# Kernel tuning notes

Measured on AMD Instinct MI355X. Metric: run time of the kernel, lower is better.

Reference implementation:

```python
import jax, jax.numpy as jnp
import numpy as np

EMBED_DIM = 768
NUM_HEADS = 12
HEAD_DIM = EMBED_DIM // NUM_HEADS
BSZ = 2
SEQ = 2048


def setup_inputs() -> dict:
    key = jax.random.key(0)
    ks = jax.random.split(key, 8)
    w = lambda k: (jax.random.normal(k, (EMBED_DIM, EMBED_DIM), jnp.float32) * 0.02)
    return {
        "hidden_states": jax.random.normal(ks[0], (BSZ, SEQ, EMBED_DIM), jnp.float32),
        "attention_mask": jnp.zeros((BSZ, 1, SEQ, SEQ), jnp.float32),
        "attention_bias": jax.random.normal(ks[1], (BSZ * NUM_HEADS, SEQ), jnp.float32),
        "Wq": w(ks[2]), "bq": jnp.zeros((EMBED_DIM,), jnp.float32),
        "Wk": w(ks[3]), "bk": jnp.zeros((EMBED_DIM,), jnp.float32),
        "Wv": w(ks[4]), "bv": jnp.zeros((EMBED_DIM,), jnp.float32),
        "Wo": w(ks[5]), "bo": jnp.zeros((EMBED_DIM,), jnp.float32),
        "beta": jnp.ones((1,), jnp.float32),
        "beta_bias": jnp.zeros((1,), jnp.float32),
    }


def reference(hidden_states, attention_mask, attention_bias, Wq, bq, Wk, bk, Wv, bv, Wo, bo, beta, beta_bias):
    b, t, e = hidden_states.shape
    scaling = HEAD_DIM ** -0.5
    split = lambda x: x.reshape(b, t, NUM_HEADS, HEAD_DIM).transpose(0, 2, 1, 3)  # b h t d
    q = split(hidden_states @ Wq.T + bq) * scaling
    k = split(hidden_states @ Wk.T + bk)
    v = split(hidden_states @ Wv.T + bv)
    # scores: [b, h, t, s]
    scores = jnp.einsum('bhqd,bhkd->bhqk', q, k)
    bias = attention_bias.reshape(b, NUM_HEADS, 1, t)  # (bsz*nh, src) -> broadcast over queries
    scores = scores + beta * bias + beta_bias + attention_mask
    probs = jax.nn.softmax(scores, axis=-1)
    out = jnp.einsum('bhqk,bhkd->bhqd', probs, v)  # b h t d
    out = out.transpose(0, 2, 1, 3).reshape(b, t, e)
    return out @ Wo.T + bo
```

## Files before the change

### kernel.cpp

```cpp
#include <hip/hip_runtime.h>
#include <hip/hip_bf16.h>

#define E 768
#define HD 64
#define NH 12
#define BSZ 2
#define SEQ 2048
#define M_ROWS (BSZ * SEQ)
#define BH (BSZ * NH)

#define LOG2E 1.44269504f
#define QSCALE 0.18033688f
#define MSHIFT 16.0f

typedef float f4_t __attribute__((ext_vector_type(4)));
typedef float f32x16 __attribute__((ext_vector_type(16)));
typedef __bf16 bf8_t __attribute__((ext_vector_type(8)));
typedef unsigned short us8_t __attribute__((ext_vector_type(8)));
typedef unsigned short us4_t __attribute__((ext_vector_type(4)));

__device__ inline unsigned short f2bf(float f) {
  union { float f; unsigned u; } v; v.f = f;
  unsigned u = v.u + 0x7FFFu + ((v.u >> 16) & 1u);
  return (unsigned short)(u >> 16);
}

__device__ inline float ex2(float x) { return __builtin_amdgcn_exp2f(x); }

__device__ inline float bflo(unsigned u) { union { unsigned u; float f; } v; v.u = u << 16; return v.f; }
__device__ inline float bfhi(unsigned u) { union { unsigned u; float f; } v; v.u = u & 0xFFFF0000u; return v.f; }

__device__ inline unsigned pk2(float a, float b) {
  union { float f; unsigned u; } ua, ub;
  ua.f = a; ub.f = b;
  return __builtin_amdgcn_perm(ub.u + 0x8000u, ua.u + 0x8000u, 0x07060302u);
}

__device__ inline void swap32(unsigned& a, unsigned& b) {
  asm volatile("v_permlane32_swap_b32 %0, %1" : "+v"(a), "+v"(b));
}

__global__ __launch_bounds__(256) void cvt_all(
    const float* __restrict__ X, const float* __restrict__ Wq,
    const float* __restrict__ Wk, const float* __restrict__ Wv,
    const float* __restrict__ Wo, const float* __restrict__ mask,
    const float* __restrict__ abias, const float* __restrict__ betaP,
    const float* __restrict__ bbiasP,
    unsigned short* __restrict__ Xbf, unsigned short* __restrict__ Wqkv,
    unsigned short* __restrict__ Wobf, unsigned short* __restrict__ maskbf,
    float* __restrict__ biasPf) {
  const int nW = E * E;
  int id = blockIdx.x;
  if (id < 2688) {
    const float* src;
    unsigned short* dst;
    float scale = 1.0f;
    int base;
    if (id < 1536) {
      src = X; dst = Xbf; base = id * 2048;
    } else {
      int r = id - 1536;
      int k = r / 288;
      int rb = r - k * 288;
      base = rb * 2048;
      if (k == 0)      { src = Wq; dst = Wqkv;          scale = QSCALE; }
      else if (k == 1) { src = Wk; dst = Wqkv + nW;     }
      else if (k == 2) { src = Wv; dst = Wqkv + 2 * nW; }
      else             { src = Wo; dst = Wobf;          }
    }
    int i = base + threadIdx.x * 8;
    const float4* s = (const float4*)(src + i);
    float4 a = s[0], b = s[1];
    us8_t o;
    o[0] = f2bf(a.x * scale); o[1] = f2bf(a.y * scale);
    o[2] = f2bf(a.z * scale); o[3] = f2bf(a.w * scale);
    o[4] = f2bf(b.x * scale); o[5] = f2bf(b.y * scale);
    o[6] = f2bf(b.z * scale); o[7] = f2bf(b.w * scale);
    *(us8_t*)(dst + i) = o;
    return;
  }
  if (id < 6784) {
    int rowid = id - 2688;
    int bb = rowid >> 11, q = rowid & 2047;
    int s0 = threadIdx.x * 8;
    const float4* s = (const float4*)(mask + (size_t)rowid * 2048 + s0);
    float4 a = s[0], c = s[1];
    int tile = s0 >> 6, kk = s0 & 63;
    int base = ((bb * 32 + tile) * 2048 + q) * 64 + (kk >> 5) * 32 + ((kk & 31) >> 3) * 4;
    us4_t lo, hi4;
    lo[0] = f2bf(a.x * LOG2E); lo[1] = f2bf(a.y * LOG2E);
    lo[2] = f2bf(a.z * LOG2E); lo[3] = f2bf(a.w * LOG2E);
    hi4[0] = f2bf(c.x * LOG2E); hi4[1] = f2bf(c.y * LOG2E);
    hi4[2] = f2bf(c.z * LOG2E); hi4[3] = f2bf(c.w * LOG2E);
    *(us4_t*)(maskbf + base) = lo;
    *(us4_t*)(maskbf + base + 16) = hi4;
    return;
  }
  {
    int bh = id - 6784;
    int s0 = threadIdx.x * 8;
    const float4* s = (const float4*)(abias + (size_t)bh * 2048 + s0);
    float4 a = s[0], c = s[1];
    float bv = LOG2E * betaP[0];
    float bc = LOG2E * bbiasP[0] - MSHIFT;
    int tile = s0 >> 6, kk = s0 & 63;
    int base = bh * 2048 + tile * 64 + (kk >> 5) * 32 + ((kk & 31) >> 3) * 4;
    f4_t lo = {fmaf(bv, a.x, bc), fmaf(bv, a.y, bc), fmaf(bv, a.z, bc), fmaf(bv, a.w, bc)};
    f4_t hi4 = {fmaf(bv, c.x, bc), fmaf(bv, c.y, bc), fmaf(bv, c.z, bc), fmaf(bv, c.w, bc)};
    *(f4_t*)(biasPf + base) = lo;
    *(f4_t*)(biasPf + base + 16) = hi4;
  }
}

__global__ __launch_bounds__(256) void gemm_qkv(
    const unsigned short* __restrict__ A, const unsigned short* __restrict__ Bw,
    const float* __restrict__ bq, const float* __restrict__ bk, const float* __restrict__ bv,
    unsigned short* __restrict__ Qb, unsigned short* __restrict__ Kb,
    unsigned short* __restrict__ Vtb) {
  __shared__ unsigned short Alds[2][64 * 64];
  __shared__ unsigned short Blds[2][128 * 64];
  const int w = threadIdx.x >> 6, lane = threadIdx.x & 63;
  const int quad = lane >> 4, l15 = lane & 15;
  const int rowBase = blockIdx.x * 64;
  const int colBase = blockIdx.y * 128;
  const int wr = (w & 1) * 32, wc = (w >> 1) * 64;
  f4_t acc[2][4] = {};
  const int swz = l15 & 7;

#define STAGE_QKV(BUF, K0)                                                       \
  {                                                                              \
    const int kk0_ = (K0);                                                       \
    for (int c = 0; c < 2; ++c) {                                                \
      int s = c * 256 + w * 64 + lane;                                           \
      int r = s >> 3, col = ((s & 7) ^ (r & 7)) * 8;                             \
      const unsigned short* ga = A + (size_t)(rowBase + r) * E + kk0_ + col;     \
      __builtin_amdgcn_global_load_lds(                                          \
          (const __attribute__((address_space(1))) void*)ga,                     \
          (__attribute__((address_space(3))) void*)&Alds[BUF][c * 2048 + w * 512], 16, 0, 0); \
    }                                                                            \
    for (int c = 0; c < 4; ++c) {                                                \
      int s = c * 256 + w * 64 + lane;                                           \
      int r = s >> 3, col = ((s & 7) ^ (r & 7)) * 8;                             \
      const unsigned short* gb = Bw + (size_t)(colBase + r) * E + kk0_ + col;    \
      __builtin_amdgcn_global_load_lds(                                          \
          (const __attribute__((address_space(1))) void*)gb,                     \
          (__attribute__((address_space(3))) void*)&Blds[BUF][c * 2048 + w * 512], 16, 0, 0); \
    }                                                                            \
  }

  STAGE_QKV(0, 0);
  __builtin_amdgcn_s_waitcnt(0);
  __syncthreads();
  for (int t = 0; t < 12; ++t) {
    const int cur = t & 1;
    if (t < 11) STAGE_QKV(cur ^ 1, (t + 1) * 64);
    bf8_t af[2][2], bfr[4][2];
#pragma unroll
    for (int mi = 0; mi < 2; ++mi)
#pragma unroll
      for (int ks = 0; ks < 2; ++ks)
        af[mi][ks] = *(const bf8_t*)&Alds[cur][(wr + mi * 16 + l15) * 64 + (((ks * 4 + quad) ^ swz) << 3)];
#pragma unroll
    for (int ni = 0; ni < 4; ++ni)
#pragma unroll
      for (int ks = 0; ks < 2; ++ks)
        bfr[ni][ks] = *(const bf8_t*)&Blds[cur][(wc + ni * 16 + l15) * 64 + (((ks * 4 + quad) ^ swz) << 3)];
#pragma unroll
    for (int ks = 0; ks < 2; ++ks)
#pragma unroll
      for (int mi = 0; mi < 2; ++mi)
#pragma unroll
        for (int ni = 0; ni < 4; ++ni)
          acc[mi][ni] = __builtin_amdgcn_mfma_f32_16x16x32_bf16(af[mi][ks], bfr[ni][ks], acc[mi][ni], 0, 0, 0);
    __builtin_amdgcn_s_waitcnt(0);
    __syncthreads();
  }
#undef STAGE_QKV

  const int which = colBase / E;
  if (which < 2) {
    const float* biasP = (which == 0) ? bq : bk;
    unsigned short* dst = (which == 0) ? Qb : Kb;
    const float bscale = (which == 0) ? QSCALE : 1.0f;
    const int cnBase = colBase - which * E + wc;
    const int h = cnBase >> 6;
    float biasv[4];
#pragma unroll
    for (int ni = 0; ni < 4; ++ni) biasv[ni] = biasP[cnBase + ni * 16 + l15] * bscale;
    unsigned short* T = &Blds[0][0] + w * 1024;
    const int row = lane >> 2, colE = (lane & 3) * 16;
#pragma unroll
    for (int mi = 0; mi < 2; ++mi) {
#pragma unroll
      for (int ni = 0; ni < 4; ++ni)
#pragma unroll
        for (int r = 0; r < 4; ++r)
          T[(quad * 4 + r) * 64 + ni * 16 + l15] = f2bf(acc[mi][ni][r] + biasv[ni]);
      us8_t o0 = *(const us8_t*)&T[row * 64 + colE];
      us8_t o1 = *(const us8_t*)&T[row * 64 + colE + 8];
      int gm = rowBase + wr + mi * 16 + row;
      int b = gm >> 11, t = gm & 2047;
      unsigned short* drow = dst + ((size_t)(b * NH + h) * SEQ + t) * HD;
      *(us8_t*)&drow[colE] = o0;
      *(us8_t*)&drow[colE + 8] = o1;
    }
  } else {
#pragma unroll
    for (int mi = 0; mi < 2; ++mi) {
#pragma unroll
      for (int ni = 0; ni < 4; ++ni) {
        int cn = colBase - 2 * E + wc + ni * 16 + l15;
        int h = cn >> 6, d = cn & 63;
        float bias = bv[cn];
        int gm0 = rowBase + wr + mi * 16 + quad * 4;
        int b = gm0 >> 11, t = gm0 & 2047;
        us4_t o4;
#pragma unroll
        for (int r = 0; r < 4; ++r) o4[r] = f2bf(acc[mi][ni][r] + bias);
        *(us4_t*)&Vtb[((size_t)(b * NH + h) * HD + d) * SEQ + t] = o4;
      }
    }
  }
}

__device__ inline void initS(f32x16& SA, const float* bp, us8_t ma, us8_t mb) {
  union { us8_t s; unsigned u[4]; } ca, cb;
  ca.s = ma; cb.s = mb;
#pragma unroll
  for (int g = 0; g < 4; ++g) {
    f4_t bw = *(const f4_t*)(bp + g * 4);
    unsigned wl = (g < 2) ? ca.u[2 * g] : cb.u[2 * g - 4];
    unsigned wh = (g < 2) ? ca.u[2 * g + 1] : cb.u[2 * g - 3];
    SA[4 * g + 0] = bw[0] + bflo(wl);
    SA[4 * g + 1] = bw[1] + bfhi(wl);
    SA[4 * g + 2] = bw[2] + bflo(wh);
    SA[4 * g + 3] = bw[3] + bfhi(wh);
  }
}

__device__ inline void packP(f32x16& SA, float& L, bf8_t& F0, bf8_t& F1) {
#pragma unroll
  for (int r = 0; r < 16; ++r) {
    SA[r] = ex2(SA[r]);
    L += SA[r];
  }
  unsigned u0 = pk2(SA[0], SA[1]), u1 = pk2(SA[2], SA[3]);
  unsigned u2 = pk2(SA[4], SA[5]), u3 = pk2(SA[6], SA[7]);
  unsigned u4 = pk2(SA[8], SA[9]), u5 = pk2(SA[10], SA[11]);
  unsigned u6 = pk2(SA[12], SA[13]), u7 = pk2(SA[14], SA[15]);
  swap32(u0, u2); swap32(u1, u3); swap32(u4, u6); swap32(u5, u7);
  union { unsigned u[4]; bf8_t b; } fa, fb;
  fa.u[0] = u0; fa.u[1] = u1; fa.u[2] = u2; fa.u[3] = u3;
  fb.u[0] = u4; fb.u[1] = u5; fb.u[2] = u6; fb.u[3] = u7;
  F0 = fa.b; F1 = fb.b;
}

__global__ __launch_bounds__(256, 3) void flash_attn15(
    const unsigned short* __restrict__ Qb, const unsigned short* __restrict__ Kb,
    const unsigned short* __restrict__ Vt, const unsigned short* __restrict__ maskP,
    const float* __restrict__ biasPf, unsigned short* __restrict__ attn) {
  __shared__ __align__(16) char smem[40960];
  const int tid = threadIdx.x;
  const int w = tid >> 6, lane = tid & 63;
  const int l31 = lane & 31, hi = lane >> 5;
  const int p = w >> 1, qw = (w & 1) * 32;
  const int id = blockIdx.x;
  const int h = id >> 6;
  const int qb = id & 63;
  const int qt = qb >> 1, b = qb & 1;
  const int bh = b * NH + h;
  const int q0 = qt * 64;
  const int q = q0 + qw + l31;

  unsigned short* KldsP = (unsigned short*)(smem + p * 16384);
  unsigned short* VldsP = KldsP + 4096;
  float* biasF = (float*)(smem + 32768);

  {
    const float* srcB = biasPf + bh * 2048 + tid * 8;
    *(f4_t*)&biasF[tid * 8] = *(const f4_t*)srcB;
    *(f4_t*)&biasF[tid * 8 + 4] = *(const f4_t*)(srcB + 4);
  }

  bf8_t qf[4];
  {
    const unsigned short* qbase = Qb + ((size_t)bh * SEQ + q) * HD + hi * 8;
#pragma unroll
    for (int dk = 0; dk < 4; ++dk) qf[dk] = *(const bf8_t*)(qbase + dk * 16);
  }

  const int li = (w & 1) * 64 + lane;
  const int r0 = li >> 3, cc = li & 7;
  const int dstOff = r0 * 64 + ((cc ^ (r0 & 7)) << 3);
  const unsigned short* kb0 = Kb + (size_t)bh * SEQ * HD + (p * 1024 + r0) * 64 + cc * 8;
  const unsigned short* VtG = Vt + (size_t)bh * HD * SEQ;
  const unsigned short* vb0 = VtG + (size_t)r0 * SEQ + p * 1024 + cc * 8;
  const unsigned short* mpp = maskP + (((size_t)(b * 32 + p * 16) * 2048) + q) * 64 + hi * 16;

  us8_t kpf0, kpf1, kpf2, kpf3, vpf0, vpf1, vpf2, vpf3, mpf0, mpf1, mpf2, mpf3;

#define PF_KV()                                                               \
  asm volatile("global_load_dwordx4 %0, %8, off\n\t"                          \
               "global_load_dwordx4 %1, %8, off offset:2048\n\t"              \
               "global_load_dwordx4 %2, %9, off\n\t"                          \
               "global_load_dwordx4 %3, %9, off offset:2048\n\t"              \
               "global_load_dwordx4 %4, %10, off\n\t"                         \
               "global_load_dwordx4 %5, %11, off\n\t"                         \
               "global_load_dwordx4 %6, %12, off\n\t"                         \
               "global_load_dwordx4 %7, %13, off"                             \
               : "=&v"(kpf0), "=&v"(kpf1), "=&v"(kpf2), "=&v"(kpf3),          \
                 "=&v"(vpf0), "=&v"(vpf1), "=&v"(vpf2), "=&v"(vpf3)           \
               : "v"(kb0), "v"(kb0 + 2048), "v"(vb0), "v"(vb0 + 16 * SEQ),    \
                 "v"(vb0 + 32 * SEQ), "v"(vb0 + 48 * SEQ))

#define PF_M()                                                                \
  asm volatile("global_load_dwordx4 %0, %4, off\n\t"                          \
               "global_load_dwordx4 %1, %4, off offset:16\n\t"                \
               "global_load_dwordx4 %2, %4, off offset:64\n\t"                \
               "global_load_dwordx4 %3, %4, off offset:80"                    \
               : "=&v"(mpf0), "=&v"(mpf1), "=&v"(mpf2), "=&v"(mpf3)           \
               : "v"(mpp))

  PF_KV();
  PF_M();

  f32x16 Oacc0 = {}, Oacc1 = {};
  float Lacc = 0.0f;
  const int swzA = l31 & 7;

  for (int it = 0; it < 16; ++it) {
    asm volatile("s_waitcnt vmcnt(4)"
                 : "+v"(kpf0), "+v"(kpf1), "+v"(kpf2), "+v"(kpf3),
                   "+v"(vpf0), "+v"(vpf1), "+v"(vpf2), "+v"(vpf3));
    __syncthreads();
    {
      us8_t* kd = (us8_t*)(KldsP + dstOff);
      kd[0] = kpf0; kd[128] = kpf1; kd[256] = kpf2; kd[384] = kpf3;
      us8_t* vd = (us8_t*)(VldsP + dstOff);
      vd[0] = vpf0; vd[128] = vpf1; vd[256] = vpf2; vd[384] = vpf3;
    }
    __syncthreads();

    if (it < 15) {
      kb0 += 4096; vb0 += 64;
      PF_KV();
      asm volatile("s_waitcnt vmcnt(8)"
                   : "+v"(mpf0), "+v"(mpf1), "+v"(mpf2), "+v"(mpf3));
    } else {
      asm volatile("s_waitcnt vmcnt(0)"
                   : "+v"(mpf0), "+v"(mpf1), "+v"(mpf2), "+v"(mpf3));
    }

    const float* bp = biasF + ((p << 4) + it) * 64 + (hi << 4);
    f32x16 s0, s1;
    initS(s0, bp, mpf0, mpf1);
    initS(s1, bp + 32, mpf2, mpf3);

    if (it < 15) { mpp += 131072; PF_M(); }

    __builtin_amdgcn_s_setprio(1);
#pragma unroll
    for (int dk = 0; dk < 4; ++dk) {
      const int co = ((dk * 2 + hi) ^ swzA) << 3;
      bf8_t k0 = *(const bf8_t*)(KldsP + l31 * 64 + co);
      bf8_t k1 = *(const bf8_t*)(KldsP + (32 + l31) * 64 + co);
      s0 = __builtin_amdgcn_mfma_f32_32x32x16_bf16(k0, qf[dk], s0, 0, 0, 0);
      s1 = __builtin_amdgcn_mfma_f32_32x32x16_bf16(k1, qf[dk], s1, 0, 0, 0);
    }
    __builtin_amdgcn_s_setprio(0);

    bf8_t pfr0, pfr1, pfr2, pfr3;
    packP(s0, Lacc, pfr0, pfr1);
    packP(s1, Lacc, pfr2, pfr3);

    __builtin_amdgcn_s_setprio(1);
#pragma unroll
    for (int ks = 0; ks < 4; ++ks) {
      const int co = ((ks * 2 + hi) ^ swzA) << 3;
      bf8_t v0 = *(const bf8_t*)(VldsP + l31 * 64 + co);
      bf8_t v1 = *(const bf8_t*)(VldsP + (32 + l31) * 64 + co);
      bf8_t pp = ks == 0 ? pfr0 : ks == 1 ? pfr1 : ks == 2 ? pfr2 : pfr3;
      Oacc0 = __builtin_amdgcn_mfma_f32_32x32x16_bf16(v0, pp, Oacc0, 0, 0, 0);
      Oacc1 = __builtin_amdgcn_mfma_f32_32x32x16_bf16(v1, pp, Oacc1, 0, 0, 0);
    }
    __builtin_amdgcn_s_setprio(0);
  }
#undef PF_KV
#undef PF_M

  __syncthreads();
  {
    float* OfP = (float*)smem + p * (64 * 65);
    const int qr = (qw + l31) * 65;
#pragma unroll
    for (int r = 0; r < 16; ++r) {
      int d = (r & 3) + 8 * (r >> 2) + 4 * hi;
      OfP[qr + d] = Oacc0[r];
      OfP[qr + 32 + d] = Oacc1[r];
    }
    float Lf = Lacc + __shfl_xor(Lacc, 32);
    if (hi == 0) OfP[qr + 64] = Lf;
  }
  __syncthreads();
  {
    const float* O0 = (const float*)smem;
    const float* O1 = O0 + 64 * 65;
    const int ql = tid >> 2, dc = tid & 3;
    const int qr = ql * 65;
    float inv = 1.0f / (O0[qr + 64] + O1[qr + 64]);
    unsigned short* orow = attn + ((size_t)b * SEQ + q0 + ql) * E + h * HD + dc * 16;
    us8_t o0, o1;
#pragma unroll
    for (int i = 0; i < 8; ++i)
      o0[i] = f2bf((O0[qr + dc * 16 + i] + O1[qr + dc * 16 + i]) * inv);
#pragma unroll
    for (int i = 0; i < 8; ++i)
      o1[i] = f2bf((O0[qr + dc * 16 + 8 + i] + O1[qr + dc * 16 + 8 + i]) * inv);
    *(us8_t*)orow = o0;
    *(us8_t*)(orow + 8) = o1;
  }
}

__global__ __launch_bounds__(256) void gemm_out(
    const unsigned short* __restrict__ A, const unsigned short* __restrict__ Bw,
    const float* __restrict__ bo, float* __restrict__ out) {
  __shared__ unsigned short Alds[2][64 * 64];
  __shared__ unsigned short Blds[2][64 * 64];
  const int w = threadIdx.x >> 6, lane = threadIdx.x & 63;
  const int quad = lane >> 4, l15 = lane & 15;
  const int rowBase = blockIdx.x * 64;
  const int colBase = blockIdx.y * 64;
  const int wr = (w & 1) * 32, wc = (w >> 1) * 32;
  f4_t acc[2][2] = {};
  const int swz = l15 & 7;

#define STAGE_OUT(BUF, K0)                                                       \
  {                                                                              \
    const int kk0_ = (K0);                                                       \
    for (int c = 0; c < 2; ++c) {                                                \
      int s = c * 256 + w * 64 + lane;                                           \
      int r = s >> 3, col = ((s & 7) ^ (r & 7)) * 8;                             \
      const unsigned short* ga = A + (size_t)(rowBase + r) * E + kk0_ + col;     \
      __builtin_amdgcn_global_load_lds(                                          \
          (const __attribute__((address_space(1))) void*)ga,                     \
          (__attribute__((address_space(3))) void*)&Alds[BUF][c * 2048 + w * 512], 16, 0, 0); \
      const unsigned short* gb = Bw + (size_t)(colBase + r) * E + kk0_ + col;    \
      __builtin_amdgcn_global_load_lds(                                          \
          (const __attribute__((address_space(1))) void*)gb,                     \
          (__attribute__((address_space(3))) void*)&Blds[BUF][c * 2048 + w * 512], 16, 0, 0); \
    }                                                                            \
  }

  STAGE_OUT(0, 0);
  __builtin_amdgcn_s_waitcnt(0);
  __syncthreads();
  for (int t = 0; t < 12; ++t) {
    const int cur = t & 1;
    if (t < 11) STAGE_OUT(cur ^ 1, (t + 1) * 64);
    bf8_t af[2][2], bfr[2][2];
#pragma unroll
    for (int mi = 0; mi < 2; ++mi)
#pragma unroll
      for (int ks = 0; ks < 2; ++ks)
        af[mi][ks] = *(const bf8_t*)&Alds[cur][(wr + mi * 16 + l15) * 64 + (((ks * 4 + quad) ^ swz) << 3)];
#pragma unroll
    for (int ni = 0; ni < 2; ++ni)
#pragma unroll
      for (int ks = 0; ks < 2; ++ks)
        bfr[ni][ks] = *(const bf8_t*)&Blds[cur][(wc + ni * 16 + l15) * 64 + (((ks * 4 + quad) ^ swz) << 3)];
#pragma unroll
    for (int ks = 0; ks < 2; ++ks)
#pragma unroll
      for (int mi = 0; mi < 2; ++mi)
#pragma unroll
        for (int ni = 0; ni < 2; ++ni)
          acc[mi][ni] = __builtin_amdgcn_mfma_f32_16x16x32_bf16(af[mi][ks], bfr[ni][ks], acc[mi][ni], 0, 0, 0);
    __builtin_amdgcn_s_waitcnt(0);
    __syncthreads();
  }
#undef STAGE_OUT

#pragma unroll
  for (int mi = 0; mi < 2; ++mi) {
#pragma unroll
    for (int ni = 0; ni < 2; ++ni) {
      int gn = colBase + wc + ni * 16 + l15;
      float bias = bo[gn];
#pragma unroll
      for (int r = 0; r < 4; ++r) {
        int gm = rowBase + wr + mi * 16 + quad * 4 + r;
        out[(size_t)gm * E + gn] = acc[mi][ni][r] + bias;
      }
    }
  }
}

extern "C" void kernel_launch(void* const* d_in, const int* in_sizes, int n_in,
                              void* d_out, int out_size, void* d_ws, size_t ws_size,
                              hipStream_t stream) {
  const float* hidden = (const float*)d_in[0];
  const float* mask = (const float*)d_in[1];
  const float* abias = (const float*)d_in[2];
  const float* Wq = (const float*)d_in[3];
  const float* bq = (const float*)d_in[4];
  const float* Wk = (const float*)d_in[5];
  const float* bk = (const float*)d_in[6];
  const float* Wv = (const float*)d_in[7];
  const float* bv = (const float*)d_in[8];
  const float* Wo = (const float*)d_in[9];
  const float* bo = (const float*)d_in[10];
  const float* beta = (const float*)d_in[11];
  const float* betaBias = (const float*)d_in[12];
  float* out = (float*)d_out;

  char* ws = (char*)d_ws;
  unsigned short* Xbf = (unsigned short*)(ws);
  unsigned short* Wqkv = (unsigned short*)(ws + 6291456);
  unsigned short* Wobf = (unsigned short*)(ws + 9830400);
  unsigned short* Qbuf = (unsigned short*)(ws + 11010048);
  unsigned short* Kbuf = (unsigned short*)(ws + 17301504);
  unsigned short* Vtb = (unsigned short*)(ws + 23592960);
  unsigned short* Maskbf = (unsigned short*)(ws + 29884416);
  float* BiasP = (float*)(ws + 46661632);
  unsigned short* Attn = Xbf;

  cvt_all<<<6808, 256, 0, stream>>>(hidden, Wq, Wk, Wv, Wo, mask, abias, beta, betaBias,
                                    Xbf, Wqkv, Wobf, Maskbf, BiasP);
  gemm_qkv<<<dim3(64, 18), 256, 0, stream>>>(Xbf, Wqkv, bq, bk, bv, Qbuf, Kbuf, Vtb);
  flash_attn15<<<768, 256, 0, stream>>>(Qbuf, Kbuf, Vtb, Maskbf, BiasP, Attn);
  gemm_out<<<dim3(64, 12), 256, 0, stream>>>(Attn, Wobf, bo, out);
}
```

Measured before the change: 200.8 us.

## Enlarge GEMM tiles, drop double buffering, and tree-reduce softmax row sums

The QKV GEMM moves from 64x128 to 128x128 tiles with 4x4 MFMA accumulators per wave and a minimum of 3 blocks per CU. The output GEMM moves from 64x64 to 64x128 tiles. Both GEMMs drop LDS double buffering for a single buffer with a sync before and after each load, which reuses each loaded tile more and cuts LDS use but stops overlapping loads with MFMA work. The softmax row sum in the attention kernel now uses a tree reduction instead of a serial chain, shortening the dependency chain.

```diff
diff --git a/kernel.cpp b/kernel.cpp
--- a/kernel.cpp
+++ b/kernel.cpp
@@ -112,85 +112,72 @@
   }
 }
 
-__global__ __launch_bounds__(256) void gemm_qkv(
+__global__ __launch_bounds__(256, 3) void gemm_qkv(
     const unsigned short* __restrict__ A, const unsigned short* __restrict__ Bw,
     const float* __restrict__ bq, const float* __restrict__ bk, const float* __restrict__ bv,
     unsigned short* __restrict__ Qb, unsigned short* __restrict__ Kb,
     unsigned short* __restrict__ Vtb) {
-  __shared__ unsigned short Alds[2][64 * 64];
-  __shared__ unsigned short Blds[2][128 * 64];
+  __shared__ unsigned short Alds[128 * 64];
+  __shared__ unsigned short Blds[128 * 64];
   const int w = threadIdx.x >> 6, lane = threadIdx.x & 63;
   const int quad = lane >> 4, l15 = lane & 15;
-  const int rowBase = blockIdx.x * 64;
+  const int rowBase = blockIdx.x * 128;
   const int colBase = blockIdx.y * 128;
-  const int wr = (w & 1) * 32, wc = (w >> 1) * 64;
-  f4_t acc[2][4] = {};
+  const int wr = (w & 1) * 64, wc = (w >> 1) * 64;
+  f4_t acc[4][4] = {};
   const int swz = l15 & 7;
 
-#define STAGE_QKV(BUF, K0)                                                       \
-  {                                                                              \
-    const int kk0_ = (K0);                                                       \
-    for (int c = 0; c < 2; ++c) {                                                \
-      int s = c * 256 + w * 64 + lane;                                           \
-      int r = s >> 3, col = ((s & 7) ^ (r & 7)) * 8;                             \
-      const unsigned short* ga = A + (size_t)(rowBase + r) * E + kk0_ + col;     \
-      __builtin_amdgcn_global_load_lds(                                          \
-          (const __attribute__((address_space(1))) void*)ga,                     \
-          (__attribute__((address_space(3))) void*)&Alds[BUF][c * 2048 + w * 512], 16, 0, 0); \
-    }                                                                            \
-    for (int c = 0; c < 4; ++c) {                                                \
-      int s = c * 256 + w * 64 + lane;                                           \
-      int r = s >> 3, col = ((s & 7) ^ (r & 7)) * 8;                             \
-      const unsigned short* gb = Bw + (size_t)(colBase + r) * E + kk0_ + col;    \
-      __builtin_amdgcn_global_load_lds(                                          \
-          (const __attribute__((address_space(1))) void*)gb,                     \
-          (__attribute__((address_space(3))) void*)&Blds[BUF][c * 2048 + w * 512], 16, 0, 0); \
-    }                                                                            \
-  }
-
-  STAGE_QKV(0, 0);
-  __builtin_amdgcn_s_waitcnt(0);
-  __syncthreads();
-  for (int t = 0; t < 12; ++t) {
-    const int cur = t & 1;
-    if (t < 11) STAGE_QKV(cur ^ 1, (t + 1) * 64);
-    bf8_t af[2][2], bfr[4][2];
-#pragma unroll
-    for (int mi = 0; mi < 2; ++mi)
+  for (int k0 = 0; k0 < E; k0 += 64) {
+    __syncthreads();
+#pragma unroll
+    for (int c = 0; c < 4; ++c) {
+      int s = c * 256 + w * 64 + lane;
+      int r = s >> 3, col = ((s & 7) ^ (r & 7)) * 8;
+      const unsigned short* ga = A + (size_t)(rowBase + r) * E + k0 + col;
+      __builtin_amdgcn_global_load_lds((const __attribute__((address_space(1))) void*)ga,
+          (__attribute__((address_space(3))) void*)&Alds[c * 2048 + w * 512], 16, 0, 0);
+      const unsigned short* gb = Bw + (size_t)(colBase + r) * E + k0 + col;
+      __builtin_amdgcn_global_load_lds((const __attribute__((address_space(1))) void*)gb,
+          (__attribute__((address_space(3))) void*)&Blds[c * 2048 + w * 512], 16, 0, 0);
+    }
+    __builtin_amdgcn_s_waitcnt(0);
+    __syncthreads();
+    bf8_t af[4][2], bfr[4][2];
+#pragma unroll
+    for (int mi = 0; mi < 4; ++mi)
 #pragma unroll
       for (int ks = 0; ks < 2; ++ks)
-        af[mi][ks] = *(const bf8_t*)&Alds[cur][(wr + mi * 16 + l15) * 64 + (((ks * 4 + quad) ^ swz) << 3)];
+        af[mi][ks] = *(const bf8_t*)&Alds[(wr + mi * 16 + l15) * 64 + (((ks * 4 + quad) ^ swz) << 3)];
 #pragma unroll
     for (int ni = 0; ni < 4; ++ni)
 #pragma unroll
       for (int ks = 0; ks < 2; ++ks)
-        bfr[ni][ks] = *(const bf8_t*)&Blds[cur][(wc + ni * 16 + l15) * 64 + (((ks * 4 + quad) ^ swz) << 3)];
+        bfr[ni][ks] = *(const bf8_t*)&Blds[(wc + ni * 16 + l15) * 64 + (((ks * 4 + quad) ^ swz) << 3)];
 #pragma unroll
     for (int ks = 0; ks < 2; ++ks)
 #pragma unroll
-      for (int mi = 0; mi < 2; ++mi)
+      for (int mi = 0; mi < 4; ++mi)
 #pragma unroll
         for (int ni = 0; ni < 4; ++ni)
           acc[mi][ni] = __builtin_amdgcn_mfma_f32_16x16x32_bf16(af[mi][ks], bfr[ni][ks], acc[mi][ni], 0, 0, 0);
-    __builtin_amdgcn_s_waitcnt(0);
-    __syncthreads();
-  }
-#undef STAGE_QKV
-
-  const int which = colBase / E;
+  }
+
+  const int which = blockIdx.y / 6;
+  const int colMat = colBase - which * E;
+  __syncthreads();
   if (which < 2) {
     const float* biasP = (which == 0) ? bq : bk;
     unsigned short* dst = (which == 0) ? Qb : Kb;
     const float bscale = (which == 0) ? QSCALE : 1.0f;
-    const int cnBase = colBase - which * E + wc;
+    const int cnBase = colMat + wc;
     const int h = cnBase >> 6;
     float biasv[4];
 #pragma unroll
     for (int ni = 0; ni < 4; ++ni) biasv[ni] = biasP[cnBase + ni * 16 + l15] * bscale;
-    unsigned short* T = &Blds[0][0] + w * 1024;
+    unsigned short* T = Blds + w * 1024;
     const int row = lane >> 2, colE = (lane & 3) * 16;
 #pragma unroll
-    for (int mi = 0; mi < 2; ++mi) {
+    for (int mi = 0; mi < 4; ++mi) {
 #pragma unroll
       for (int ni = 0; ni < 4; ++ni)
 #pragma unroll
@@ -206,10 +193,10 @@
     }
   } else {
 #pragma unroll
-    for (int mi = 0; mi < 2; ++mi) {
+    for (int mi = 0; mi < 4; ++mi) {
 #pragma unroll
       for (int ni = 0; ni < 4; ++ni) {
-        int cn = colBase - 2 * E + wc + ni * 16 + l15;
+        int cn = colMat + wc + ni * 16 + l15;
         int h = cn >> 6, d = cn & 63;
         float bias = bv[cn];
         int gm0 = rowBase + wr + mi * 16 + quad * 4;
@@ -240,10 +227,12 @@
 
 __device__ inline void packP(f32x16& SA, float& L, bf8_t& F0, bf8_t& F1) {
 #pragma unroll
-  for (int r = 0; r < 16; ++r) {
-    SA[r] = ex2(SA[r]);
-    L += SA[r];
-  }
+  for (int r = 0; r < 16; ++r) SA[r] = ex2(SA[r]);
+  float t0 = (SA[0] + SA[1]) + (SA[2] + SA[3]);
+  float t1 = (SA[4] + SA[5]) + (SA[6] + SA[7]);
+  float t2 = (SA[8] + SA[9]) + (SA[10] + SA[11]);
+  float t3 = (SA[12] + SA[13]) + (SA[14] + SA[15]);
+  L += (t0 + t1) + (t2 + t3);
   unsigned u0 = pk2(SA[0], SA[1]), u1 = pk2(SA[2], SA[3]);
   unsigned u2 = pk2(SA[4], SA[5]), u3 = pk2(SA[6], SA[7]);
   unsigned u4 = pk2(SA[8], SA[9]), u5 = pk2(SA[10], SA[11]);
@@ -255,7 +244,7 @@
   F0 = fa.b; F1 = fb.b;
 }
 
-__global__ __launch_bounds__(256, 3) void flash_attn15(
+__global__ __launch_bounds__(256, 3) void flash_attn16(
     const unsigned short* __restrict__ Qb, const unsigned short* __restrict__ Kb,
     const unsigned short* __restrict__ Vt, const unsigned short* __restrict__ maskP,
     const float* __restrict__ biasPf, unsigned short* __restrict__ attn) {
@@ -424,66 +413,60 @@
 __global__ __launch_bounds__(256) void gemm_out(
     const unsigned short* __restrict__ A, const unsigned short* __restrict__ Bw,
     const float* __restrict__ bo, float* __restrict__ out) {
-  __shared__ unsigned short Alds[2][64 * 64];
-  __shared__ unsigned short Blds[2][64 * 64];
+  __shared__ unsigned short Alds[64 * 64];
+  __shared__ unsigned short Blds[128 * 64];
   const int w = threadIdx.x >> 6, lane = threadIdx.x & 63;
   const int quad = lane >> 4, l15 = lane & 15;
   const int rowBase = blockIdx.x * 64;
-  const int colBase = blockIdx.y * 64;
-  const int wr = (w & 1) * 32, wc = (w >> 1) * 32;
-  f4_t acc[2][2] = {};
+  const int colBase = blockIdx.y * 128;
+  const int wr = (w & 1) * 32, wc = (w >> 1) * 64;
+  f4_t acc[2][4] = {};
   const int swz = l15 & 7;
 
-#define STAGE_OUT(BUF, K0)                                                       \
-  {                                                                              \
-    const int kk0_ = (K0);                                                       \
-    for (int c = 0; c < 2; ++c) {                                                \
-      int s = c * 256 + w * 64 + lane;                                           \
-      int r = s >> 3, col = ((s & 7) ^ (r & 7)) * 8;                             \
-      const unsigned short* ga = A + (size_t)(rowBase + r) * E + kk0_ + col;     \
-      __builtin_amdgcn_global_load_lds(                                          \
-          (const __attribute__((address_space(1))) void*)ga,                     \
-          (__attribute__((address_space(3))) void*)&Alds[BUF][c * 2048 + w * 512], 16, 0, 0); \
-      const unsigned short* gb = Bw + (size_t)(colBase + r) * E + kk0_ + col;    \
-      __builtin_amdgcn_global_load_lds(                                          \
-          (const __attribute__((address_space(1))) void*)gb,                     \
-          (__attribute__((address_space(3))) void*)&Blds[BUF][c * 2048 + w * 512], 16, 0, 0); \
-    }                                                                            \
-  }
-
-  STAGE_OUT(0, 0);
-  __builtin_amdgcn_s_waitcnt(0);
-  __syncthreads();
-  for (int t = 0; t < 12; ++t) {
-    const int cur = t & 1;
-    if (t < 11) STAGE_OUT(cur ^ 1, (t + 1) * 64);
-    bf8_t af[2][2], bfr[2][2];
-#pragma unroll
-    for (int mi = 0; mi < 2; ++mi)
-#pragma unroll
-      for (int ks = 0; ks < 2; ++ks)
-        af[mi][ks] = *(const bf8_t*)&Alds[cur][(wr + mi * 16 + l15) * 64 + (((ks * 4 + quad) ^ swz) << 3)];
-#pragma unroll
-    for (int ni = 0; ni < 2; ++ni)
-#pragma unroll
-      for (int ks = 0; ks < 2; ++ks)
-        bfr[ni][ks] = *(const bf8_t*)&Blds[cur][(wc + ni * 16 + l15) * 64 + (((ks * 4 + quad) ^ swz) << 3)];
-#pragma unroll
-    for (int ks = 0; ks < 2; ++ks)
-#pragma unroll
-      for (int mi = 0; mi < 2; ++mi)
-#pragma unroll
-        for (int ni = 0; ni < 2; ++ni)
-          acc[mi][ni] = __builtin_amdgcn_mfma_f32_16x16x32_bf16(af[mi][ks], bfr[ni][ks], acc[mi][ni], 0, 0, 0);
+  for (int k0 = 0; k0 < E; k0 += 64) {
+    __syncthreads();
+#pragma unroll
+    for (int c = 0; c < 2; ++c) {
+      int s = c * 256 + w * 64 + lane;
+      int r = s >> 3, col = ((s & 7) ^ (r & 7)) * 8;
+      const unsigned short* ga = A + (size_t)(rowBase + r) * E + k0 + col;
+      __builtin_amdgcn_global_load_lds((const __attribute__((address_space(1))) void*)ga,
+          (__attribute__((address_space(3))) void*)&Alds[c * 2048 + w * 512], 16, 0, 0);
+    }
+#pragma unroll
+    for (int c = 0; c < 4; ++c) {
+      int s = c * 256 + w * 64 + lane;
+      int r = s >> 3, col = ((s & 7) ^ (r & 7)) * 8;
+      const unsigned short* gb = Bw + (size_t)(colBase + r) * E + k0 + col;
+      __builtin_amdgcn_global_load_lds((const __attribute__((address_space(1))) void*)gb,
+          (__attribute__((address_space(3))) void*)&Blds[c * 2048 + w * 512], 16, 0, 0);
+    }
     __builtin_amdgcn_s_waitcnt(0);
     __syncthreads();
-  }
-#undef STAGE_OUT
+    bf8_t af[2][2], bfr[4][2];
+#pragma unroll
+    for (int mi = 0; mi < 2; ++mi)
+#pragma unroll
+      for (int ks = 0; ks < 2; ++ks)
+        af[mi][ks] = *(const bf8_t*)&Alds[(wr + mi * 16 + l15) * 64 + (((ks * 4 + quad) ^ swz) << 3)];
+#pragma unroll
+    for (int ni = 0; ni < 4; ++ni)
+#pragma unroll
+      for (int ks = 0; ks < 2; ++ks)
+        bfr[ni][ks] = *(const bf8_t*)&Blds[(wc + ni * 16 + l15) * 64 + (((ks * 4 + quad) ^ swz) << 3)];
+#pragma unroll
+    for (int ks = 0; ks < 2; ++ks)
+#pragma unroll
+      for (int mi = 0; mi < 2; ++mi)
+#pragma unroll
+        for (int ni = 0; ni < 4; ++ni)
+          acc[mi][ni] = __builtin_amdgcn_mfma_f32_16x16x32_bf16(af[mi][ks], bfr[ni][ks], acc[mi][ni], 0, 0, 0);
+  }
 
 #pragma unroll
   for (int mi = 0; mi < 2; ++mi) {
 #pragma unroll
-    for (int ni = 0; ni < 2; ++ni) {
+    for (int ni = 0; ni < 4; ++ni) {
       int gn = colBase + wc + ni * 16 + l15;
       float bias = bo[gn];
 #pragma unroll
@@ -526,7 +509,7 @@
 
   cvt_all<<<6808, 256, 0, stream>>>(hidden, Wq, Wk, Wv, Wo, mask, abias, beta, betaBias,
                                     Xbf, Wqkv, Wobf, Maskbf, BiasP);
-  gemm_qkv<<<dim3(64, 18), 256, 0, stream>>>(Xbf, Wqkv, bq, bk, bv, Qbuf, Kbuf, Vtb);
-  flash_attn15<<<768, 256, 0, stream>>>(Qbuf, Kbuf, Vtb, Maskbf, BiasP, Attn);
-  gemm_out<<<dim3(64, 12), 256, 0, stream>>>(Attn, Wobf, bo, out);
-}
+  gemm_qkv<<<dim3(32, 18), 256, 0, stream>>>(Xbf, Wqkv, bq, bk, bv, Qbuf, Kbuf, Vtb);
+  flash_attn16<<<768, 256, 0, stream>>>(Qbuf, Kbuf, Vtb, Maskbf, BiasP, Attn);
+  gemm_out<<<dim3(64, 6), 256, 0, stream>>>(Attn, Wobf, bo, out);
+}
```

Measured after the change: 196.2 us. 1.02x faster.
